# Optimization experiments

Measured on AMD Instinct MI355X. Metric: run time of the kernel, lower is better.

Reference implementation:

```python
import math
import jax, jax.numpy as jnp
import numpy as np

MAX_LEN = 2048
D_HEAD = 64
B, H, S = 4, 16, 1024


def setup_inputs() -> dict:
    key = jax.random.key(0)
    kq, kk, kp = jax.random.split(key, 3)
    q = jax.random.normal(kq, (B, H, S, D_HEAD), dtype=jnp.float32)
    k = jax.random.normal(kk, (B, H, S, D_HEAD), dtype=jnp.float32)
    pos_table = jax.random.normal(kp, (MAX_LEN, D_HEAD), dtype=jnp.float32)
    return {"q": q, "k": k, "pos_table": pos_table}


def reference(q, k, pos_table):
    d_head = q.shape[-1]
    seq_len = q.shape[2]
    max_len = pos_table.shape[0]
    scale = 1.0 / math.sqrt(d_head)
    # attention gates: (b,h,s,s)
    gates = jax.nn.sigmoid(jnp.einsum('bhsd,bhtd->bhst', q, k) * scale)
    # context positions: weighted sum of key indices -> (b,h,s)
    positions = jnp.arange(seq_len, dtype=q.dtype)
    ctx_pos = jnp.einsum('bhst,t->bhs', gates, positions)
    ctx_pos = jnp.clip(ctx_pos, 0.0, float(max_len - 2))
    pos_floor = ctx_pos.astype(jnp.int32)  # (b,h,s)
    pos_frac = (ctx_pos - pos_floor.astype(q.dtype))[..., None]  # (b,h,s,1)
    emb_floor = pos_table[pos_floor]  # (b,h,s,d)
    emb_ceil = pos_table[jnp.minimum(pos_floor + 1, max_len - 1)]
    pos_emb = emb_floor + pos_frac * (emb_ceil - emb_floor)  # (b,h,s,d)
    # bias: (b,h,s,s)
    bias = jnp.einsum('bhsd,bhtd->bhst', q, pos_emb)
    return bias
```

## Files before the change

### kernel.cpp

```cpp
#include <hip/hip_runtime.h>

#define Bb_ 4
#define Hh_ 16
#define Ss_ 1024
#define DH 64
#define MAXLEN 2048
#define BH (Bb_*Hh_)
#define LDST 72
#define SW 132

typedef __attribute__((ext_vector_type(8))) short short8;
typedef __attribute__((ext_vector_type(4))) float floatx4;
typedef __attribute__((ext_vector_type(4))) unsigned short ushort4v;

static __device__ __forceinline__ unsigned short f2bf(float f) {
    unsigned int u = __builtin_bit_cast(unsigned int, f);
    u = (u + 0x7fffu + ((u >> 16) & 1u)) >> 16;
    return (unsigned short)u;
}

static __device__ __forceinline__ void stage_tile(unsigned short* lds,
                                                  const float* __restrict__ g,
                                                  int tid) {
#pragma unroll
    for (int it = 0; it < 8; ++it) {
        int idx = it * 1024 + tid * 4;
        int row = idx >> 6, col = idx & 63;
        const float4 v = *reinterpret_cast<const float4*>(g + row * 64 + col);
        ushort4v o = { f2bf(v.x), f2bf(v.y), f2bf(v.z), f2bf(v.w) };
        *reinterpret_cast<ushort4v*>(lds + row * LDST + col) = o;
    }
}

__global__ __launch_bounds__(256, 2)
void ctx_kernel(const float* __restrict__ q, const float* __restrict__ k,
                float* __restrict__ ctx) {
    __shared__ __align__(16) unsigned short Ab[128 * LDST];
    __shared__ __align__(16) unsigned short Kb[128 * LDST];

    int bx = blockIdx.x;
    int bh = bx >> 3, mt = bx & 7;
    int m0 = mt << 7;
    int tid = threadIdx.x;
    int lane = tid & 63, w = tid >> 6;
    int lo = lane & 15, quad = lane >> 4;

    stage_tile(Ab, q + (size_t)(bh * Ss_ + m0) * DH, tid);
    __syncthreads();

    short8 afr[2][2];
#pragma unroll
    for (int i = 0; i < 2; ++i)
#pragma unroll
        for (int k2 = 0; k2 < 2; ++k2)
            afr[i][k2] = *reinterpret_cast<const short8*>(
                &Ab[(w * 32 + i * 16 + lo) * LDST + k2 * 32 + quad * 8]);

    float rp[2][4];
#pragma unroll
    for (int i = 0; i < 2; ++i)
#pragma unroll
        for (int r = 0; r < 4; ++r) rp[i][r] = 0.f;

    for (int tt = 0; tt < 8; ++tt) {
        int t0 = tt << 7;
        __syncthreads();
        stage_tile(Kb, k + (size_t)(bh * Ss_ + t0) * DH, tid);
        __syncthreads();

#pragma unroll
        for (int j = 0; j < 8; ++j) {
            short8 b0 = *reinterpret_cast<const short8*>(
                &Kb[(j * 16 + lo) * LDST + 0 + quad * 8]);
            short8 b1 = *reinterpret_cast<const short8*>(
                &Kb[(j * 16 + lo) * LDST + 32 + quad * 8]);
            float tcol = (float)(t0 + j * 16 + lo);
#pragma unroll
            for (int i = 0; i < 2; ++i) {
                floatx4 c = {0.f, 0.f, 0.f, 0.f};
                c = __builtin_amdgcn_mfma_f32_16x16x32_bf16(afr[i][0], b0, c, 0, 0, 0);
                c = __builtin_amdgcn_mfma_f32_16x16x32_bf16(afr[i][1], b1, c, 0, 0, 0);
#pragma unroll
                for (int r = 0; r < 4; ++r) {
                    float x = c[r] * 0.125f;
                    float e = __expf(-x);
                    float g = __builtin_amdgcn_rcpf(1.0f + e);
                    rp[i][r] += g * tcol;
                }
            }
        }
    }

#pragma unroll
    for (int i = 0; i < 2; ++i)
#pragma unroll
        for (int r = 0; r < 4; ++r) {
            float v = rp[i][r];
            v += __shfl_xor(v, 1);
            v += __shfl_xor(v, 2);
            v += __shfl_xor(v, 4);
            v += __shfl_xor(v, 8);
            rp[i][r] = v;
        }

    if (lo == 0) {
#pragma unroll
        for (int i = 0; i < 2; ++i)
#pragma unroll
            for (int r = 0; r < 4; ++r) {
                int row = m0 + w * 32 + i * 16 + quad * 4 + r;
                float v = fminf(fmaxf(rp[i][r], 0.f), (float)(MAXLEN - 2));
                ctx[bh * Ss_ + row] = v;
            }
    }
}

__global__ __launch_bounds__(256, 4)
void bias_kernel(const float* __restrict__ q, const float* __restrict__ tb,
                 const float* __restrict__ ctx, float* __restrict__ out) {
    __shared__ __align__(16) unsigned char smem[2 * 128 * LDST * 2];
    unsigned short* Ab = reinterpret_cast<unsigned short*>(smem);
    unsigned short* Pb = Ab + 128 * LDST;
    float* scratch = reinterpret_cast<float*>(smem);

    int bx = blockIdx.x;
    int bh = bx >> 6;
    int mt = (bx >> 3) & 7;
    int nt = bx & 7;
    int m0 = mt << 7, n0 = nt << 7;
    int tid = threadIdx.x;
    int lane = tid & 63, w = tid >> 6;
    int lo = lane & 15, quad = lane >> 4;

    stage_tile(Ab, q + (size_t)(bh * Ss_ + m0) * DH, tid);

    {
        int rsub = tid >> 4;
        int d0 = (tid & 15) * 4;
#pragma unroll
        for (int pass = 0; pass < 8; ++pass) {
            int row = pass * 16 + rsub;
            float c = ctx[bh * Ss_ + n0 + row];
            int fl = (int)c;
            float fr = c - (float)fl;
            int ce = min(fl + 1, MAXLEN - 1);
            const float4 e0 = *reinterpret_cast<const float4*>(tb + fl * DH + d0);
            const float4 e1 = *reinterpret_cast<const float4*>(tb + ce * DH + d0);
            ushort4v o = { f2bf(e0.x + fr * (e1.x - e0.x)),
                           f2bf(e0.y + fr * (e1.y - e0.y)),
                           f2bf(e0.z + fr * (e1.z - e0.z)),
                           f2bf(e0.w + fr * (e1.w - e0.w)) };
            *reinterpret_cast<ushort4v*>(&Pb[row * LDST + d0]) = o;
        }
    }
    __syncthreads();

    short8 afr[2][2];
#pragma unroll
    for (int i = 0; i < 2; ++i)
#pragma unroll
        for (int k2 = 0; k2 < 2; ++k2)
            afr[i][k2] = *reinterpret_cast<const short8*>(
                &Ab[(w * 32 + i * 16 + lo) * LDST + k2 * 32 + quad * 8]);

    floatx4 acc[2][8];
#pragma unroll
    for (int i = 0; i < 2; ++i)
#pragma unroll
        for (int j = 0; j < 8; ++j) acc[i][j] = (floatx4){0.f, 0.f, 0.f, 0.f};

#pragma unroll
    for (int j = 0; j < 8; ++j) {
        short8 b0 = *reinterpret_cast<const short8*>(
            &Pb[(j * 16 + lo) * LDST + 0 + quad * 8]);
        short8 b1 = *reinterpret_cast<const short8*>(
            &Pb[(j * 16 + lo) * LDST + 32 + quad * 8]);
#pragma unroll
        for (int i = 0; i < 2; ++i) {
            acc[i][j] = __builtin_amdgcn_mfma_f32_16x16x32_bf16(afr[i][0], b0, acc[i][j], 0, 0, 0);
            acc[i][j] = __builtin_amdgcn_mfma_f32_16x16x32_bf16(afr[i][1], b1, acc[i][j], 0, 0, 0);
        }
    }

#pragma unroll
    for (int i = 0; i < 2; ++i) {
        __syncthreads();
#pragma unroll
        for (int j = 0; j < 8; ++j)
#pragma unroll
            for (int r = 0; r < 4; ++r) {
                int lrow = w * 16 + quad * 4 + r;
                scratch[lrow * SW + j * 16 + lo] = acc[i][j][r];
            }
        __syncthreads();
#pragma unroll
        for (int it = 0; it < 8; ++it) {
            int flat = it * 1024 + tid * 4;
            int lrow = flat >> 7, col = flat & 127;
            floatx4 v = *reinterpret_cast<const floatx4*>(&scratch[lrow * SW + col]);
            int grow = m0 + (lrow >> 4) * 32 + i * 16 + (lrow & 15);
            __builtin_nontemporal_store(
                v, reinterpret_cast<floatx4*>(
                       out + (size_t)(bh * Ss_ + grow) * Ss_ + n0 + col));
        }
    }
}

extern "C" void kernel_launch(void* const* d_in, const int* in_sizes, int n_in,
                              void* d_out, int out_size, void* d_ws, size_t ws_size,
                              hipStream_t stream) {
    const float* q  = (const float*)d_in[0];
    const float* k  = (const float*)d_in[1];
    const float* tb = (const float*)d_in[2];
    float* ctx = (float*)d_ws;
    float* out = (float*)d_out;

    ctx_kernel<<<BH * 8, 256, 0, stream>>>(q, k, ctx);
    bias_kernel<<<BH * 64, 256, 0, stream>>>(q, tb, ctx, out);
}
```

Baseline: 323.6 us.

## Add uniform-context fast path that writes row-constant bias without MFMA

ctx_kernel now also reduces the min and max of the clipped context positions for each 128-row tile into a small workspace array. bias_kernel reads these per (batch, head), and when all positions in the head are equal it takes a fast path. That path builds one interpolated embedding row, computes an fp32 dot product per query row, and broadcasts that value across the output tile. This skips the bf16 staging, embedding gather and MFMA work whenever the sigmoid-weighted sum saturates the clip. That is the usual case for these inputs, though the check is exact in general. The cost is an extra shared-memory reduction and sync in ctx_kernel, plus 8 small loads per bias block.

```diff
diff --git a/kernel.cpp b/kernel.cpp
--- a/kernel.cpp
+++ b/kernel.cpp
@@ -34,9 +34,10 @@
 
 __global__ __launch_bounds__(256, 2)
 void ctx_kernel(const float* __restrict__ q, const float* __restrict__ k,
-                float* __restrict__ ctx) {
+                float* __restrict__ ctx, float2* __restrict__ mm) {
     __shared__ __align__(16) unsigned short Ab[128 * LDST];
     __shared__ __align__(16) unsigned short Kb[128 * LDST];
+    __shared__ float sh_ctx[128];
 
     int bx = blockIdx.x;
     int bh = bx >> 3, mt = bx & 7;
@@ -108,20 +109,31 @@
         for (int i = 0; i < 2; ++i)
 #pragma unroll
             for (int r = 0; r < 4; ++r) {
-                int row = m0 + w * 32 + i * 16 + quad * 4 + r;
+                int lr = w * 32 + i * 16 + quad * 4 + r;
                 float v = fminf(fmaxf(rp[i][r], 0.f), (float)(MAXLEN - 2));
-                ctx[bh * Ss_ + row] = v;
-            }
+                sh_ctx[lr] = v;
+                ctx[bh * Ss_ + m0 + lr] = v;
+            }
+    }
+    __syncthreads();
+
+    if (tid < 64) {
+        float a = sh_ctx[tid], b = sh_ctx[tid + 64];
+        float mn = fminf(a, b), mx = fmaxf(a, b);
+#pragma unroll
+        for (int off = 1; off < 64; off <<= 1) {
+            mn = fminf(mn, __shfl_xor(mn, off));
+            mx = fmaxf(mx, __shfl_xor(mx, off));
+        }
+        if (tid == 0) mm[bh * 8 + mt] = make_float2(mn, mx);
     }
 }
 
 __global__ __launch_bounds__(256, 4)
 void bias_kernel(const float* __restrict__ q, const float* __restrict__ tb,
-                 const float* __restrict__ ctx, float* __restrict__ out) {
+                 const float* __restrict__ ctx, const float2* __restrict__ mm,
+                 float* __restrict__ out) {
     __shared__ __align__(16) unsigned char smem[2 * 128 * LDST * 2];
-    unsigned short* Ab = reinterpret_cast<unsigned short*>(smem);
-    unsigned short* Pb = Ab + 128 * LDST;
-    float* scratch = reinterpret_cast<float*>(smem);
 
     int bx = blockIdx.x;
     int bh = bx >> 6;
@@ -131,6 +143,66 @@
     int tid = threadIdx.x;
     int lane = tid & 63, w = tid >> 6;
     int lo = lane & 15, quad = lane >> 4;
+
+    float mn = 3.0e38f, mx = -3.0e38f;
+#pragma unroll
+    for (int j = 0; j < 8; ++j) {
+        float2 p = mm[bh * 8 + j];
+        mn = fminf(mn, p.x);
+        mx = fmaxf(mx, p.y);
+    }
+
+    if (mn == mx) {
+        float* pr = reinterpret_cast<float*>(smem);
+        float* sc = pr + 64;
+
+        float v = mn;
+        int fl = (int)v;
+        float fr = v - (float)fl;
+        int ce = min(fl + 1, MAXLEN - 1);
+        if (tid < 16) {
+            int d0 = tid * 4;
+            const float4 e0 = *reinterpret_cast<const float4*>(tb + fl * DH + d0);
+            const float4 e1 = *reinterpret_cast<const float4*>(tb + ce * DH + d0);
+            pr[d0 + 0] = e0.x + fr * (e1.x - e0.x);
+            pr[d0 + 1] = e0.y + fr * (e1.y - e0.y);
+            pr[d0 + 2] = e0.z + fr * (e1.z - e0.z);
+            pr[d0 + 3] = e0.w + fr * (e1.w - e0.w);
+        }
+        __syncthreads();
+
+        {
+            int row = tid >> 1, half = tid & 1;
+            const float* qr = q + (size_t)(bh * Ss_ + m0 + row) * DH + half * 32;
+            const float* ph = pr + half * 32;
+            float s = 0.f;
+#pragma unroll
+            for (int d = 0; d < 32; d += 4) {
+                const float4 qq = *reinterpret_cast<const float4*>(qr + d);
+                s += qq.x * ph[d] + qq.y * ph[d + 1] + qq.z * ph[d + 2] +
+                     qq.w * ph[d + 3];
+            }
+            s += __shfl_xor(s, 1);
+            if (half == 0) sc[row] = s;
+        }
+        __syncthreads();
+
+#pragma unroll
+        for (int it = 0; it < 16; ++it) {
+            int flat = (it * 256 + tid) * 4;
+            int lrow = flat >> 7, col = flat & 127;
+            float c = sc[lrow];
+            floatx4 vv = {c, c, c, c};
+            __builtin_nontemporal_store(
+                vv, reinterpret_cast<floatx4*>(
+                        out + (size_t)(bh * Ss_ + m0 + lrow) * Ss_ + n0 + col));
+        }
+        return;
+    }
+
+    unsigned short* Ab = reinterpret_cast<unsigned short*>(smem);
+    unsigned short* Pb = Ab + 128 * LDST;
+    float* scratch = reinterpret_cast<float*>(smem);
 
     stage_tile(Ab, q + (size_t)(bh * Ss_ + m0) * DH, tid);
 
@@ -197,11 +269,11 @@
         for (int it = 0; it < 8; ++it) {
             int flat = it * 1024 + tid * 4;
             int lrow = flat >> 7, col = flat & 127;
-            floatx4 v = *reinterpret_cast<const floatx4*>(&scratch[lrow * SW + col]);
+            floatx4 vv = *reinterpret_cast<const floatx4*>(&scratch[lrow * SW + col]);
             int grow = m0 + (lrow >> 4) * 32 + i * 16 + (lrow & 15);
             __builtin_nontemporal_store(
-                v, reinterpret_cast<floatx4*>(
-                       out + (size_t)(bh * Ss_ + grow) * Ss_ + n0 + col));
+                vv, reinterpret_cast<floatx4*>(
+                        out + (size_t)(bh * Ss_ + grow) * Ss_ + n0 + col));
         }
     }
 }
@@ -213,8 +285,9 @@
     const float* k  = (const float*)d_in[1];
     const float* tb = (const float*)d_in[2];
     float* ctx = (float*)d_ws;
+    float2* mm = (float2*)((float*)d_ws + BH * Ss_);
     float* out = (float*)d_out;
 
-    ctx_kernel<<<BH * 8, 256, 0, stream>>>(q, k, ctx);
-    bias_kernel<<<BH * 64, 256, 0, stream>>>(q, tb, ctx, out);
-}
+    ctx_kernel<<<BH * 8, 256, 0, stream>>>(q, k, ctx, mm);
+    bias_kernel<<<BH * 64, 256, 0, stream>>>(q, tb, ctx, mm, out);
+}
```

Result: no change. 327.4 us (+1.2%).
